# Performance work log

Hardware: AMD Instinct MI355X
Metric: run time of the kernel (lower is better)

Reference implementation:

```python
import math
import jax, jax.numpy as jnp
import numpy as np

D_MODEL = 512
N_HEADS = 8
FACTOR = 1
B, L = 16, 2048


def setup_inputs() -> dict:
    key = jax.random.key(0)
    ks = jax.random.split(key, 12)
    d = D_MODEL
    inp = {
        'queries': jax.random.normal(ks[0], (B, L, d), dtype=jnp.float32),
        'keys':    jax.random.normal(ks[1], (B, L, d), dtype=jnp.float32),
        'values':  jax.random.normal(ks[2], (B, L, d), dtype=jnp.float32),
        # projection params (nn.Linear: y = x @ W.T + b)
        'Wq': jax.random.normal(ks[3], (d, d), dtype=jnp.float32) * 0.02,
        'bq': jnp.zeros((d,), dtype=jnp.float32),
        'Wk': jax.random.normal(ks[4], (d, d), dtype=jnp.float32) * 0.02,
        'bk': jnp.zeros((d,), dtype=jnp.float32),
        'Wv': jax.random.normal(ks[5], (d, d), dtype=jnp.float32) * 0.02,
        'bv': jnp.zeros((d,), dtype=jnp.float32),
        'Wo': jax.random.normal(ks[6], (d, d), dtype=jnp.float32) * 0.02,
        'bo': jnp.zeros((d,), dtype=jnp.float32),
    }
    return inp


def _autocorrelation(q, k, v):
    # q, k, v: [B, H, E, L]
    length = q.shape[-1]
    q_fft = jnp.fft.rfft(q, axis=-1)
    k_fft = jnp.fft.rfft(k, axis=-1)
    corr = jnp.fft.irfft(q_fft * jnp.conj(k_fft), n=length, axis=-1)  # [B,H,E,L]

    # time_delay_agg_training
    top_k = int(FACTOR * math.log(length))  # static
    mean_value = corr.mean(axis=(1, 2))            # [B, L]
    _, index = jax.lax.top_k(mean_value.mean(axis=0), top_k)  # [k], batch-shared delays
    weights = mean_value[:, index]                 # [B, k]
    tmp_corr = jax.nn.softmax(weights, axis=-1)    # [B, k]

    # roll(values, -delay) == values[..., (arange(L)+delay) % L]
    idx = (jnp.arange(length)[None, :] + index[:, None]) % length  # [k, L]
    patterns = v[..., idx]                         # [B, H, E, k, L]
    delays_agg = jnp.einsum('bhekl,bk->bhel', patterns, tmp_corr)  # [B,H,E,L]
    return delays_agg


def reference(queries, keys, values, Wq, bq, Wk, bk, Wv, bv, Wo, bo):
    Bb, Ll, d = queries.shape
    H = N_HEADS
    E = d // H
    # projections, then [B, L, H, E] -> [B, H, E, L]
    q = (queries @ Wq.T + bq).reshape(Bb, Ll, H, E).transpose(0, 2, 3, 1)
    k = (keys    @ Wk.T + bk).reshape(Bb, Ll, H, E).transpose(0, 2, 3, 1)
    v = (values  @ Wv.T + bv).reshape(Bb, Ll, H, E).transpose(0, 2, 3, 1)

    agg = _autocorrelation(q, k, v)                 # [B, H, E, L]
    out = agg.transpose(0, 3, 1, 2).reshape(Bb, Ll, H * E)  # [B, L, d]
    return out @ Wo.T + bo
```

## Files before the change

kernel.cpp:

```cpp
#include <hip/hip_runtime.h>


typedef _Float16 f16;
typedef _Float16 f16x8 __attribute__((ext_vector_type(8)));
typedef _Float16 f16x4 __attribute__((ext_vector_type(4)));
typedef float    f32x4 __attribute__((ext_vector_type(4)));

#define PSI(i) ((i) + ((i) >> 3))
#define TWI(j) ((j) + ((j) >> 4))

__device__ __forceinline__ float2 f2add(float2 a, float2 b) { return make_float2(a.x + b.x, a.y + b.y); }
__device__ __forceinline__ float2 f2sub(float2 a, float2 b) { return make_float2(a.x - b.x, a.y - b.y); }
__device__ __forceinline__ float2 cmul(float2 a, float2 b)  { return make_float2(a.x * b.x - a.y * b.y, a.x * b.y + a.y * b.x); }

__global__ __launch_bounds__(256) void cvt_weights(
    const float* __restrict__ w0, const float* __restrict__ w1,
    const float* __restrict__ w2, const float* __restrict__ w3,
    f16* __restrict__ o0, f16* __restrict__ o1, f16* __restrict__ o2, f16* __restrict__ o3)
{
    const float* src = (blockIdx.y == 0) ? w0 : (blockIdx.y == 1) ? w1 : (blockIdx.y == 2) ? w2 : w3;
    f16*         dst = (blockIdx.y == 0) ? o0 : (blockIdx.y == 1) ? o1 : (blockIdx.y == 2) ? o2 : o3;
    const int i = blockIdx.x * 256 + threadIdx.x;
    float4 val = ((const float4*)src)[i];
    f16x4 h = { (f16)val.x, (f16)val.y, (f16)val.z, (f16)val.w };
    ((f16x4*)dst)[i] = h;
}

__device__ __forceinline__ void stage_f16(const f16* __restrict__ G, int row0, int k0,
                                          f16* __restrict__ lds, int tid)
{
#pragma unroll
    for (int q = 0; q < 4; ++q) {
        const int r = q * 64 + (tid >> 3);
        const int u = (tid & 7) ^ ((tid >> 3) & 7);
        const f16* g = G + (size_t)(row0 + r) * 512 + k0 + u * 8;
        f16* d = lds + q * 4096 + (tid >> 6) * 512;
        __builtin_amdgcn_global_load_lds(
            (const __attribute__((address_space(1))) void*)g,
            (__attribute__((address_space(3))) void*)d, 16, 0, 0);
    }
}

__device__ __forceinline__ void load_f32_slab(const float* __restrict__ G, int row0, int k0,
                                              int tid, float4* __restrict__ rg)
{
#pragma unroll
    for (int q = 0; q < 4; ++q) {
        const float* g = G + (size_t)(row0 + q * 64 + (tid >> 3)) * 512 + k0 + (tid & 7) * 8;
        rg[2 * q]     = *(const float4*)g;
        rg[2 * q + 1] = *(const float4*)(g + 4);
    }
}
__device__ __forceinline__ void write_f16_slab(f16* __restrict__ lds, int tid,
                                               const float4* __restrict__ rg)
{
#pragma unroll
    for (int q = 0; q < 4; ++q) {
        float4 a = rg[2 * q], b = rg[2 * q + 1];
        f16x8 h = { (f16)a.x, (f16)a.y, (f16)a.z, (f16)a.w,
                    (f16)b.x, (f16)b.y, (f16)b.z, (f16)b.w };
        const int uu = (tid & 7) ^ ((tid >> 3) & 7);
        *(f16x8*)(lds + q * 4096 + (tid >> 3) * 64 + (uu << 3)) = h;
    }
}

template<int AF32, int BF32, int F16OUT, int MT_L2, int NT_L2, int SWZ, int SPLITB>
__global__ __launch_bounds__(512, 2) void gemm_nt(
    const void* __restrict__ A0v, const void* __restrict__ B0v, const void* __restrict__ B1v,
    void* __restrict__ Cout, int N,
    const float* __restrict__ bias_q, const float* __restrict__ bias_k,
    const float* __restrict__ bias_col)
{
    constexpr int BM = 256, BN = 256, NKT = 8;
    constexpr int ESZ = F16OUT ? 2 : 4;

    __shared__ __align__(16) char smem[131072];
    f16* smA = (f16*)smem;
    f16* smB = (f16*)smem + 2 * BM * 64;

    const int tid  = threadIdx.x;
    const int wave = tid >> 6, lane = tid & 63;

    int mt, nt;
    if (SWZ == 1) {
        const int xcd = blockIdx.x & 7, slot = blockIdx.x >> 3;
        mt = slot & ((1 << MT_L2) - 1);
        nt = (xcd << (NT_L2 - 3)) | (slot >> MT_L2);
    } else if (SWZ == 2) {
        const int xcd = blockIdx.x & 7, slot = blockIdx.x >> 3;
        nt = slot & ((1 << NT_L2) - 1);
        mt = (xcd << (MT_L2 - 3)) | (slot >> NT_L2);
    } else {
        nt = blockIdx.x & ((1 << NT_L2) - 1);
        mt = blockIdx.x >> NT_L2;
    }
    const int m0 = mt * BM, n0 = nt * BN;

    const bool useB1 = SPLITB && (mt >= (1 << (MT_L2 - 1)));
    const void* Bgv = useB1 ? B1v : B0v;
    const float* brow = SPLITB
        ? (useB1 ? bias_k - (1 << (MT_L2 - 1)) * BM : bias_q)
        : bias_q;

    const f16*   Ah = (const f16*)A0v;
    const float* Af = (const float*)A0v;
    const f16*   Bh = (const f16*)Bgv;
    const float* Bf = (const float*)Bgv;

    f32x4 acc[8][4];
#pragma unroll
    for (int m = 0; m < 8; ++m)
#pragma unroll
        for (int n = 0; n < 4; ++n) acc[m][n] = (f32x4){0.f, 0.f, 0.f, 0.f};

    const int fr = lane & 15;
    const int kg = (lane >> 4) * 8;
    const int rowm = fr & 7;
    const int wr = wave >> 2;
    const int wc = wave & 3;
    const int warow = wr * 128 + fr;
    const int wbrow = wc * 64 + fr;

    auto compute = [&](const f16* __restrict__ Ab, const f16* __restrict__ Bb) {
#pragma unroll
        for (int k2 = 0; k2 < 2; ++k2) {
            const int kb = k2 * 32 + kg;
            const int col = ((kb >> 3) ^ rowm) << 3;
            f16x8 af[8], bf[4];
#pragma unroll
            for (int m = 0; m < 8; ++m) af[m] = *(const f16x8*)&Ab[(warow + m * 16) * 64 + col];
#pragma unroll
            for (int n = 0; n < 4; ++n) bf[n] = *(const f16x8*)&Bb[(wbrow + n * 16) * 64 + col];
#pragma unroll
            for (int m = 0; m < 8; ++m)
#pragma unroll
                for (int n = 0; n < 4; ++n)
                    acc[m][n] = __builtin_amdgcn_mfma_f32_16x16x32_f16(af[m], bf[n], acc[m][n], 0, 0, 0);
        }
    };

    float4 ra[8], rb[8];

    if (AF32) { load_f32_slab(Af, m0, 0, tid, ra); write_f16_slab(smA, tid, ra); }
    else      stage_f16(Ah, m0, 0, smA, tid);
    if (BF32) { load_f32_slab(Bf, n0, 0, tid, rb); write_f16_slab(smB, tid, rb); }
    else      stage_f16(Bh, n0, 0, smB, tid);
    asm volatile("s_waitcnt vmcnt(0) lgkmcnt(0)" ::: "memory");
    __builtin_amdgcn_s_barrier();

#pragma unroll 1
    for (int kk = 0; kk < NKT; ++kk) {
        const int cur = kk & 1;
        if (kk < NKT - 1) {
            const int k0 = (kk + 1) * 64;
            if (AF32) load_f32_slab(Af, m0, k0, tid, ra);
            else      stage_f16(Ah, m0, k0, smA + (cur ^ 1) * BM * 64, tid);
            if (BF32) load_f32_slab(Bf, n0, k0, tid, rb);
            else      stage_f16(Bh, n0, k0, smB + (cur ^ 1) * BN * 64, tid);
        }
        compute(smA + cur * BM * 64, smB + cur * BN * 64);
        if (kk < NKT - 1) {
            if (AF32) write_f16_slab(smA + (cur ^ 1) * BM * 64, tid, ra);
            if (BF32) write_f16_slab(smB + (cur ^ 1) * BN * 64, tid, rb);
        }
        asm volatile("s_waitcnt vmcnt(0) lgkmcnt(0)" ::: "memory");
        __builtin_amdgcn_s_barrier();
    }

    constexpr int L     = F16OUT ? 3 : 2;
    constexpr int CPR   = (BN * ESZ) / 16;
    constexpr int HROWS = F16OUT ? 256 : 128;
    constexpr int NH    = F16OUT ? 1 : 2;
#pragma unroll 1
    for (int h = 0; h < NH; ++h) {
        __syncthreads();
        if (F16OUT || wr == h) {
            const int lr0 = wr * 128 + ((lane >> 4) << 2);
#pragma unroll
            for (int m = 0; m < 8; ++m)
#pragma unroll
                for (int n = 0; n < 4; ++n) {
                    const int col = wc * 64 + n * 16 + fr;
                    const float bc = bias_col ? bias_col[n0 + col] : 0.f;
#pragma unroll
                    for (int j = 0; j < 4; ++j) {
                        const int row  = lr0 + m * 16 + j;
                        const int rl   = row - h * HROWS * (F16OUT ? 0 : 1);
                        const int scol = ((((col >> L) ^ (row & 7)) << L) | (col & ((1 << L) - 1)));
                        float v = acc[m][n][j] + bc + (brow ? brow[m0 + row] : 0.f);
                        if (F16OUT) ((f16*)smem)[row * BN + scol] = (f16)v;
                        else        ((float*)smem)[rl * BN + scol] = v;
                    }
                }
        }
        __syncthreads();
        const int chunks = HROWS * CPR;
#pragma unroll 1
        for (int i = tid; i < chunks; i += 512) {
            const int rl  = i / CPR;
            const int u   = i % CPR;
            const int row = h * HROWS + rl;
            int4 vv = *(const int4*)(smem + (rl * CPR + (u ^ (row & 7))) * 16);
            *(int4*)((char*)Cout + ((size_t)(m0 + row) * N + n0) * ESZ + u * 16) = vv;
        }
    }
}

template<int S>
__device__ __forceinline__ void fft_pass2(float2* __restrict__ z, const float2* __restrict__ tw, int tid)
{
    constexpr int m = 1024 >> S;
    constexpr int h = m >> 1;
#pragma unroll
    for (int rep = 0; rep < 2; ++rep) {
        const int idx = tid + rep * 256;
        const int j2  = idx & (h - 1);
        const int blk = idx >> (9 - S);
        const int i   = (blk << (11 - S)) + j2;
        const float2 w1 = tw[TWI(j2 << S)];
        const float2 w2 = tw[TWI(j2 << (S + 1))];
        float2 a = z[PSI(i)], b = z[PSI(i + h)], c = z[PSI(i + m)], d = z[PSI(i + m + h)];
        float2 a1 = f2add(a, c);
        float2 c1 = cmul(f2sub(a, c), w1);
        float2 b1 = f2add(b, d);
        float2 t0 = cmul(f2sub(b, d), w1);
        float2 d1 = make_float2(t0.y, -t0.x);
        z[PSI(i)]         = f2add(a1, b1);
        z[PSI(i + h)]     = cmul(f2sub(a1, b1), w2);
        z[PSI(i + m)]     = f2add(c1, d1);
        z[PSI(i + m + h)] = cmul(f2sub(c1, d1), w2);
    }
    __syncthreads();
}

__device__ __forceinline__ void fft_tail_scatter(float2* __restrict__ z, int tid)
{
    float2 v[8];
    const int p0 = tid * 8;
#pragma unroll
    for (int e = 0; e < 8; ++e) v[e] = z[PSI(p0 + e)];
    __syncthreads();
    constexpr float RS = 0.70710678118654752f;
    const float2 W8[4] = { {1.f, 0.f}, {RS, -RS}, {0.f, -1.f}, {-RS, -RS} };
#pragma unroll
    for (int e = 0; e < 4; ++e) {
        float2 t = f2sub(v[e], v[e + 4]);
        v[e]     = f2add(v[e], v[e + 4]);
        v[e + 4] = cmul(t, W8[e]);
    }
#pragma unroll
    for (int base = 0; base < 8; base += 4) {
        float2 t0 = f2sub(v[base], v[base + 2]);
        v[base]     = f2add(v[base], v[base + 2]);
        v[base + 2] = t0;
        float2 t1 = f2sub(v[base + 1], v[base + 3]);
        v[base + 1] = f2add(v[base + 1], v[base + 3]);
        v[base + 3] = make_float2(t1.y, -t1.x);
    }
#pragma unroll
    for (int base = 0; base < 8; base += 2) {
        float2 t = f2sub(v[base], v[base + 1]);
        v[base]     = f2add(v[base], v[base + 1]);
        v[base + 1] = t;
    }
    const int br8t = (int)(__brev((unsigned)tid) >> 24);
    const int BR3[8] = {0, 4, 2, 6, 1, 5, 3, 7};
#pragma unroll
    for (int e = 0; e < 8; ++e) {
        const int f = br8t + (BR3[e] << 8);
        z[PSI(f)] = v[e];
    }
    __syncthreads();
}

__device__ __forceinline__ void fft2048_natural(float2* __restrict__ z, const float2* __restrict__ tw, int tid)
{
    fft_pass2<0>(z, tw, tid);
    fft_pass2<2>(z, tw, tid);
    fft_pass2<4>(z, tw, tid);
    fft_pass2<6>(z, tw, tid);
    fft_tail_scatter(z, tid);
}

__device__ __forceinline__ void fill_tw(float2* __restrict__ tw, int tid)
{
    for (int j = tid; j < 1024; j += 256) {
        float sv, cv;
        sincospif(-(float)j * (1.0f / 1024.0f), &sv, &cv);
        tw[TWI(j)] = make_float2(cv, sv);
    }
}

__global__ __launch_bounds__(256) void fft_corr(
    const f16* __restrict__ Qt, const f16* __restrict__ Kt,
    float2* __restrict__ Sp)
{
    __shared__ float2 z[2304];
    __shared__ float2 tw[1088];
    const int tid = threadIdx.x;
    const int grp = blockIdx.x;
    const int b   = blockIdx.y;

    fill_tw(tw, tid);
    float2 racc[5];
#pragma unroll
    for (int r = 0; r < 5; ++r) racc[r] = make_float2(0.f, 0.f);
    __syncthreads();

    for (int ch = 0; ch < 8; ++ch) {
        const int c = grp * 8 + ch;
        const f16x8* qr = (const f16x8*)(Qt + ((size_t)c * 16 + b) * 2048);
        const f16x8* kr = (const f16x8*)(Kt + ((size_t)c * 16 + b) * 2048);
        f16x8 qv = qr[tid], kv = kr[tid];
        const int e0 = tid * 8;
#pragma unroll
        for (int j = 0; j < 8; ++j)
            z[PSI(e0 + j)] = make_float2((float)qv[j], (float)kv[j]);
        __syncthreads();
        fft2048_natural(z, tw, tid);
#pragma unroll
        for (int r = 0; r < 5; ++r) {
            const int f = tid + (r << 8);
            if (f <= 1024) {
                const int pf = (2048 - f) & 2047;
                float2 Zf  = z[PSI(f)];
                float2 Zc0 = z[PSI(pf)];
                float qx = 0.5f * (Zf.x + Zc0.x), qy = 0.5f * (Zf.y - Zc0.y);
                float dx = Zf.x - Zc0.x,          dy = Zf.y + Zc0.y;
                float kx = 0.5f * dy,             ky = -0.5f * dx;
                racc[r].x += qx * kx + qy * ky;
                racc[r].y += qy * kx - qx * ky;
            }
        }
        __syncthreads();
    }
    float2* out = Sp + ((size_t)b * 64 + grp) * 1025;
#pragma unroll
    for (int r = 0; r < 5; ++r) {
        const int f = tid + (r << 8);
        if (f <= 1024) out[f] = racc[r];
    }
}

__global__ __launch_bounds__(256) void reduce_sp(
    const float2* __restrict__ Sp, float2* __restrict__ Sred)
{
    const int b = blockIdx.x;
    const int f = blockIdx.y * 256 + threadIdx.x;
    if (f > 1024) return;
    const float2* base = Sp + (size_t)b * 64 * 1025 + f;
    float sx = 0.f, sy = 0.f;
#pragma unroll 8
    for (int g = 0; g < 64; ++g) {
        float2 p = base[(size_t)g * 1025];
        sx += p.x; sy += p.y;
    }
    Sred[b * 1025 + f] = make_float2(sx, sy);
}

__global__ __launch_bounds__(256) void ifft_mean(
    const float2* __restrict__ Sred, float* __restrict__ mv)
{
    __shared__ float2 z[2304];
    __shared__ float2 tw[1088];
    const int tid = threadIdx.x;
    const int b   = blockIdx.x;
    fill_tw(tw, tid);
#pragma unroll
    for (int r = 0; r < 5; ++r) {
        const int f = tid + (r << 8);
        if (f <= 1024) {
            float2 s = Sred[b * 1025 + f];
            z[PSI(f)] = make_float2(s.x, -s.y);
            if (f >= 1 && f <= 1023)
                z[PSI(2048 - f)] = make_float2(s.x, s.y);
        }
    }
    __syncthreads();
    fft2048_natural(z, tw, tid);
    const float scale = 1.0f / (2048.0f * 512.0f);
    for (int t = tid; t < 2048; t += 256)
        mv[(size_t)b * 2048 + t] = z[PSI(t)].x * scale;
}

__global__ __launch_bounds__(256) void select_topk(
    const float* __restrict__ mv, int* __restrict__ sel, float* __restrict__ wsm)
{
    __shared__ float u[2048];
    __shared__ float rv[256];
    __shared__ int   ri[256];
    __shared__ int   ssel[7];
    const int tid = threadIdx.x;
    for (int t = tid; t < 2048; t += 256) {
        float s = 0.f;
        for (int b = 0; b < 16; ++b) s += mv[b * 2048 + t];
        u[t] = s;
    }
    __syncthreads();
    for (int k = 0; k < 7; ++k) {
        float best = -3.4e38f; int bi = 0x7fffffff;
        for (int t = tid; t < 2048; t += 256)
            if (u[t] > best) { best = u[t]; bi = t; }
        rv[tid] = best; ri[tid] = bi;
        __syncthreads();
        for (int off = 128; off > 0; off >>= 1) {
            if (tid < off) {
                if (rv[tid + off] > rv[tid] ||
                    (rv[tid + off] == rv[tid] && ri[tid + off] < ri[tid])) {
                    rv[tid] = rv[tid + off]; ri[tid] = ri[tid + off];
                }
            }
            __syncthreads();
        }
        if (tid == 0) { ssel[k] = ri[0]; sel[k] = ri[0]; u[ri[0]] = -3.4e38f; }
        __syncthreads();
    }
    if (tid < 16) {
        float vals[7], mx = -3.4e38f;
        for (int k = 0; k < 7; ++k) { vals[k] = mv[tid * 2048 + ssel[k]]; mx = fmaxf(mx, vals[k]); }
        float se = 0.f;
        for (int k = 0; k < 7; ++k) { vals[k] = expf(vals[k] - mx); se += vals[k]; }
        for (int k = 0; k < 7; ++k) wsm[tid * 7 + k] = vals[k] / se;
    }
}

__global__ __launch_bounds__(256) void aggregate(
    const f16* __restrict__ V, const int* __restrict__ sel,
    const float* __restrict__ wsm, f16* __restrict__ agg)
{
    __shared__ int   sidx[7];
    __shared__ float sw[7];
    const int bl = blockIdx.x;
    const int b = bl >> 11, l = bl & 2047;
    if (threadIdx.x < 7) { sidx[threadIdx.x] = sel[threadIdx.x]; sw[threadIdx.x] = wsm[b * 7 + threadIdx.x]; }
    __syncthreads();
    const int c = threadIdx.x;
    float a0 = 0.f, a1 = 0.f;
#pragma unroll
    for (int k = 0; k < 7; ++k) {
        const int lk = (l + sidx[k]) & 2047;
        const f16* row = V + ((size_t)b * 2048 + lk) * 512;
        a0 += sw[k] * (float)row[c];
        a1 += sw[k] * (float)row[c + 256];
    }
    f16* orow = agg + ((size_t)b * 2048 + l) * 512;
    orow[c]       = (f16)a0;
    orow[c + 256] = (f16)a1;
}

extern "C" void kernel_launch(void* const* d_in, const int* in_sizes, int n_in,
                              void* d_out, int out_size, void* d_ws, size_t ws_size,
                              hipStream_t stream)
{
    (void)in_sizes; (void)n_in; (void)out_size; (void)ws_size;
    const float* queries = (const float*)d_in[0];
    const float* keys    = (const float*)d_in[1];
    const float* values  = (const float*)d_in[2];
    const float* Wq = (const float*)d_in[3];
    const float* bq = (const float*)d_in[4];
    const float* Wk = (const float*)d_in[5];
    const float* bk = (const float*)d_in[6];
    const float* Wv = (const float*)d_in[7];
    const float* bv = (const float*)d_in[8];
    const float* Wo = (const float*)d_in[9];
    const float* bo = (const float*)d_in[10];

    char* p = (char*)d_ws;
    f16*    QKt = (f16*)p;    p += 67108864;
    f16*    Vb  = (f16*)p;    p += 33554432;
    f16*    agg = (f16*)p;    p += 33554432;
    f16*    wqh = (f16*)p;    p += 524288;
    f16*    wkh = (f16*)p;    p += 524288;
    f16*    wvh = (f16*)p;    p += 524288;
    f16*    woh = (f16*)p;    p += 524288;
    float2* Sp  = (float2*)p; p += 8396800;
    float2* Srd = (float2*)p; p += 131200;
    float*  mv  = (float*)p;  p += 131072;
    int*    sel = (int*)p;    p += 256;
    float*  wsm = (float*)p;  p += 512;
    f16*    Kt  = QKt + (size_t)512 * 32768;

    cvt_weights<<<dim3(256, 4), 256, 0, stream>>>(Wq, Wk, Wv, Wo, wqh, wkh, wvh, woh);

    gemm_nt<0, 1, 1, 2, 7, 1, 1><<<512, 512, 0, stream>>>(
        wqh, queries, keys, QKt, 32768, bq, bk, nullptr);

    gemm_nt<1, 0, 1, 7, 1, 2, 0><<<256, 512, 0, stream>>>(
        values, wvh, nullptr, Vb, 512, nullptr, nullptr, bv);

    fft_corr<<<dim3(64, 16), 256, 0, stream>>>(QKt, Kt, Sp);
    reduce_sp<<<dim3(16, 5), 256, 0, stream>>>(Sp, Srd);
    ifft_mean<<<16, 256, 0, stream>>>(Srd, mv);
    select_topk<<<1, 256, 0, stream>>>(mv, sel, wsm);
    aggregate<<<32768, 256, 0, stream>>>(Vb, sel, wsm, agg);

    gemm_nt<0, 0, 0, 7, 1, 2, 0><<<256, 512, 0, stream>>>(
        agg, woh, nullptr, (float*)d_out, 512, nullptr, nullptr, bo);
}
```

Baseline: 285.7 us.

## Fuse delay aggregation into output GEMM A-staging and widen FFT grid

The separate aggregate kernel and its f16 intermediate buffer are removed; the output projection GEMM now builds its A tiles directly by gathering seven rolled V rows per tile row, weighting them and writing f16 into LDS. This avoids writing and re-reading the 32 MB agg buffer and drops a kernel launch, at the cost of seven gathered loads per A element inside the GEMM loop. Separately, fft_corr processes 4 channels per block with twice as many blocks, doubling the partial-spectrum buffer and reduce work, to raise parallelism.

```diff
diff --git a/kernel.cpp b/kernel.cpp
--- a/kernel.cpp
+++ b/kernel.cpp
@@ -64,12 +64,38 @@
     }
 }
 
-template<int AF32, int BF32, int F16OUT, int MT_L2, int NT_L2, int SWZ, int SPLITB>
+__device__ __forceinline__ void stage_agg(const f16* __restrict__ Vb_, int l0, int k0,
+                                          const int* __restrict__ ssel, const float* __restrict__ sw,
+                                          f16* __restrict__ lds, int tid)
+{
+    const f16* base = Vb_ + k0 + (tid & 7) * 8;
+#pragma unroll
+    for (int q = 0; q < 4; ++q) {
+        const int l  = l0 + q * 64 + (tid >> 3);
+        const int uu = (tid & 7) ^ ((tid >> 3) & 7);
+        float a0 = 0.f, a1 = 0.f, a2 = 0.f, a3 = 0.f, a4 = 0.f, a5 = 0.f, a6 = 0.f, a7 = 0.f;
+#pragma unroll
+        for (int k = 0; k < 7; ++k) {
+            const int lk = (l + ssel[k]) & 2047;
+            f16x8 v = *(const f16x8*)(base + (size_t)lk * 512);
+            const float w = sw[k];
+            a0 += w * (float)v[0]; a1 += w * (float)v[1];
+            a2 += w * (float)v[2]; a3 += w * (float)v[3];
+            a4 += w * (float)v[4]; a5 += w * (float)v[5];
+            a6 += w * (float)v[6]; a7 += w * (float)v[7];
+        }
+        f16x8 h = { (f16)a0, (f16)a1, (f16)a2, (f16)a3, (f16)a4, (f16)a5, (f16)a6, (f16)a7 };
+        *(f16x8*)(lds + q * 4096 + (tid >> 3) * 64 + (uu << 3)) = h;
+    }
+}
+
+template<int AF32, int BF32, int AGG, int F16OUT, int MT_L2, int NT_L2, int SWZ, int SPLITB>
 __global__ __launch_bounds__(512, 2) void gemm_nt(
     const void* __restrict__ A0v, const void* __restrict__ B0v, const void* __restrict__ B1v,
     void* __restrict__ Cout, int N,
     const float* __restrict__ bias_q, const float* __restrict__ bias_k,
-    const float* __restrict__ bias_col)
+    const float* __restrict__ bias_col,
+    const int* __restrict__ selp, const float* __restrict__ wsmp)
 {
     constexpr int BM = 256, BN = 256, NKT = 8;
     constexpr int ESZ = F16OUT ? 2 : 4;
@@ -107,6 +133,18 @@
     const f16*   Bh = (const f16*)Bgv;
     const float* Bf = (const float*)Bgv;
 
+    int   ssel[7];
+    float sw[7];
+    const f16* Vbase = nullptr;
+    int l0 = 0;
+    if (AGG) {
+        const int b = m0 >> 11;
+        l0 = m0 & 2047;
+        Vbase = Ah + (size_t)b * 2048 * 512;
+#pragma unroll
+        for (int k = 0; k < 7; ++k) { ssel[k] = selp[k]; sw[k] = wsmp[b * 7 + k]; }
+    }
+
     f32x4 acc[8][4];
 #pragma unroll
     for (int m = 0; m < 8; ++m)
@@ -141,8 +179,9 @@
 
     float4 ra[8], rb[8];
 
-    if (AF32) { load_f32_slab(Af, m0, 0, tid, ra); write_f16_slab(smA, tid, ra); }
-    else      stage_f16(Ah, m0, 0, smA, tid);
+    if (AGG)       stage_agg(Vbase, l0, 0, ssel, sw, smA, tid);
+    else if (AF32) { load_f32_slab(Af, m0, 0, tid, ra); write_f16_slab(smA, tid, ra); }
+    else           stage_f16(Ah, m0, 0, smA, tid);
     if (BF32) { load_f32_slab(Bf, n0, 0, tid, rb); write_f16_slab(smB, tid, rb); }
     else      stage_f16(Bh, n0, 0, smB, tid);
     asm volatile("s_waitcnt vmcnt(0) lgkmcnt(0)" ::: "memory");
@@ -153,8 +192,9 @@
         const int cur = kk & 1;
         if (kk < NKT - 1) {
             const int k0 = (kk + 1) * 64;
-            if (AF32) load_f32_slab(Af, m0, k0, tid, ra);
-            else      stage_f16(Ah, m0, k0, smA + (cur ^ 1) * BM * 64, tid);
+            if (AGG)       stage_agg(Vbase, l0, k0, ssel, sw, smA + (cur ^ 1) * BM * 64, tid);
+            else if (AF32) load_f32_slab(Af, m0, k0, tid, ra);
+            else           stage_f16(Ah, m0, k0, smA + (cur ^ 1) * BM * 64, tid);
             if (BF32) load_f32_slab(Bf, n0, k0, tid, rb);
             else      stage_f16(Bh, n0, k0, smB + (cur ^ 1) * BN * 64, tid);
         }
@@ -307,8 +347,8 @@
     for (int r = 0; r < 5; ++r) racc[r] = make_float2(0.f, 0.f);
     __syncthreads();
 
-    for (int ch = 0; ch < 8; ++ch) {
-        const int c = grp * 8 + ch;
+    for (int ch = 0; ch < 4; ++ch) {
+        const int c = grp * 4 + ch;
         const f16x8* qr = (const f16x8*)(Qt + ((size_t)c * 16 + b) * 2048);
         const f16x8* kr = (const f16x8*)(Kt + ((size_t)c * 16 + b) * 2048);
         f16x8 qv = qr[tid], kv = kr[tid];
@@ -334,7 +374,7 @@
         }
         __syncthreads();
     }
-    float2* out = Sp + ((size_t)b * 64 + grp) * 1025;
+    float2* out = Sp + ((size_t)b * 128 + grp) * 1025;
 #pragma unroll
     for (int r = 0; r < 5; ++r) {
         const int f = tid + (r << 8);
@@ -348,10 +388,10 @@
     const int b = blockIdx.x;
     const int f = blockIdx.y * 256 + threadIdx.x;
     if (f > 1024) return;
-    const float2* base = Sp + (size_t)b * 64 * 1025 + f;
+    const float2* base = Sp + (size_t)b * 128 * 1025 + f;
     float sx = 0.f, sy = 0.f;
 #pragma unroll 8
-    for (int g = 0; g < 64; ++g) {
+    for (int g = 0; g < 128; ++g) {
         float2 p = base[(size_t)g * 1025];
         sx += p.x; sy += p.y;
     }
@@ -424,30 +464,6 @@
     }
 }
 
-__global__ __launch_bounds__(256) void aggregate(
-    const f16* __restrict__ V, const int* __restrict__ sel,
-    const float* __restrict__ wsm, f16* __restrict__ agg)
-{
-    __shared__ int   sidx[7];
-    __shared__ float sw[7];
-    const int bl = blockIdx.x;
-    const int b = bl >> 11, l = bl & 2047;
-    if (threadIdx.x < 7) { sidx[threadIdx.x] = sel[threadIdx.x]; sw[threadIdx.x] = wsm[b * 7 + threadIdx.x]; }
-    __syncthreads();
-    const int c = threadIdx.x;
-    float a0 = 0.f, a1 = 0.f;
-#pragma unroll
-    for (int k = 0; k < 7; ++k) {
-        const int lk = (l + sidx[k]) & 2047;
-        const f16* row = V + ((size_t)b * 2048 + lk) * 512;
-        a0 += sw[k] * (float)row[c];
-        a1 += sw[k] * (float)row[c + 256];
-    }
-    f16* orow = agg + ((size_t)b * 2048 + l) * 512;
-    orow[c]       = (f16)a0;
-    orow[c + 256] = (f16)a1;
-}
-
 extern "C" void kernel_launch(void* const* d_in, const int* in_sizes, int n_in,
                               void* d_out, int out_size, void* d_ws, size_t ws_size,
                               hipStream_t stream)
@@ -468,12 +484,11 @@
     char* p = (char*)d_ws;
     f16*    QKt = (f16*)p;    p += 67108864;
     f16*    Vb  = (f16*)p;    p += 33554432;
-    f16*    agg = (f16*)p;    p += 33554432;
     f16*    wqh = (f16*)p;    p += 524288;
     f16*    wkh = (f16*)p;    p += 524288;
     f16*    wvh = (f16*)p;    p += 524288;
     f16*    woh = (f16*)p;    p += 524288;
-    float2* Sp  = (float2*)p; p += 8396800;
+    float2* Sp  = (float2*)p; p += 16793600;
     float2* Srd = (float2*)p; p += 131200;
     float*  mv  = (float*)p;  p += 131072;
     int*    sel = (int*)p;    p += 256;
@@ -482,18 +497,17 @@
 
     cvt_weights<<<dim3(256, 4), 256, 0, stream>>>(Wq, Wk, Wv, Wo, wqh, wkh, wvh, woh);
 
-    gemm_nt<0, 1, 1, 2, 7, 1, 1><<<512, 512, 0, stream>>>(
-        wqh, queries, keys, QKt, 32768, bq, bk, nullptr);
-
-    gemm_nt<1, 0, 1, 7, 1, 2, 0><<<256, 512, 0, stream>>>(
-        values, wvh, nullptr, Vb, 512, nullptr, nullptr, bv);
-
-    fft_corr<<<dim3(64, 16), 256, 0, stream>>>(QKt, Kt, Sp);
+    gemm_nt<0, 1, 0, 1, 2, 7, 1, 1><<<512, 512, 0, stream>>>(
+        wqh, queries, keys, QKt, 32768, bq, bk, nullptr, nullptr, nullptr);
+
+    gemm_nt<1, 0, 0, 1, 7, 1, 2, 0><<<256, 512, 0, stream>>>(
+        values, wvh, nullptr, Vb, 512, nullptr, nullptr, bv, nullptr, nullptr);
+
+    fft_corr<<<dim3(128, 16), 256, 0, stream>>>(QKt, Kt, Sp);
     reduce_sp<<<dim3(16, 5), 256, 0, stream>>>(Sp, Srd);
     ifft_mean<<<16, 256, 0, stream>>>(Srd, mv);
     select_topk<<<1, 256, 0, stream>>>(mv, sel, wsm);
-    aggregate<<<32768, 256, 0, stream>>>(Vb, sel, wsm, agg);
-
-    gemm_nt<0, 0, 0, 7, 1, 2, 0><<<256, 512, 0, stream>>>(
-        agg, woh, nullptr, (float*)d_out, 512, nullptr, nullptr, bo);
-}
+
+    gemm_nt<0, 0, 1, 0, 7, 1, 2, 0><<<256, 512, 0, stream>>>(
+        Vb, woh, nullptr, (float*)d_out, 512, nullptr, nullptr, bo, sel, wsm);
+}
```

New measurement: 264.9 us (median of 2 runs). 1.08x faster.
